# Kernel tuning notes

Hardware: AMD Instinct MI355X
Metric: run time of the kernel (lower is better)

The kernel has to match this reference:

```python
import jax, jax.numpy as jnp
import numpy as np

L, T, F, DIM = 16, 16384, 2, 3
N_MIN, N_MAX = 16.0, 512.0
N_PTS = 262144
# torch code builds np.int32 primes [1, 2654435761, 805459861]; 2654435761 wraps to -1640531535.
# Since T is a power of two, int32 wraparound multiply/xor followed by nonnegative mod T gives
# bit-identical indices to the int64 torch computation.
PIS = jnp.array([1, -1640531535, 805459861], dtype=jnp.int32)
# corner ordering from get_indices: corner k = a*4+b*2+c with a->dim0, b->dim1, c->dim2
OFFS = jnp.array([[(k >> 2) & 1, (k >> 1) & 1, k & 1] for k in range(8)], dtype=jnp.float32)  # (8,3)


def setup_inputs() -> dict:
    key = jax.random.key(0)
    k1, k2 = jax.random.split(key)
    x = jax.random.uniform(k1, (N_PTS, DIM), dtype=jnp.float32)
    # nn.init.uniform_(weight, a=-1e-4, b=1e-4) for each of L tables of shape (T, F)
    embeddings = jax.random.uniform(k2, (L, T, F), minval=-1e-4, maxval=1e-4, dtype=jnp.float32)
    return {"x": x, "embeddings": embeddings}


def reference(x, embeddings):
    # per-level growth factor b = exp((log Nmax - log Nmin)/L); N_l = Nmin * b**l
    b = jnp.exp((jnp.log(N_MAX) - jnp.log(N_MIN)) / L)
    N_l = N_MIN * b ** jnp.arange(L, dtype=jnp.float32)                      # (L,)
    un_x = x[None, :, :] * N_l[:, None, None]                                # (L,N,3)  (mu=0, sigma=1)
    lo = jnp.floor(un_x)
    hi = jnp.ceil(un_x)
    d = hi - lo                                                              # (L,N,3)
    nz = d != 0
    diff = jnp.where(nz, (un_x - lo) / jnp.where(nz, d, 1.0), 0.0)           # (L,N,3)

    mask = OFFS.astype(bool)[None, None]                                     # (1,1,8,3)
    corners = jnp.where(mask, hi[:, :, None, :], lo[:, :, None, :])          # (L,N,8,3)
    ci = corners.astype(jnp.int32)
    prod = ci * PIS                                                          # (L,N,8,3) wrapping int32 mul
    idx = jnp.mod(prod[..., 0] ^ prod[..., 1] ^ prod[..., 2], T)             # (L,N,8)

    # per-level table gather: (L,T,F)[ (L,N,8) ] -> (L,N,8,F)
    feats = jax.vmap(lambda emb, i: emb[i])(embeddings, idx)

    # trilinear weights: prod over dims of (diff if corner bit else 1-diff)
    w = jnp.prod(jnp.where(mask, diff[:, :, None, :], 1.0 - diff[:, :, None, :]), axis=-1)  # (L,N,8)
    c = jnp.einsum('lnc,lncf->lnf', w, feats)                                # (L,N,F)
    return jnp.transpose(c, (1, 0, 2)).reshape(x.shape[0], L * F)            # (N, L*F)
```

## Files before the change

kernel.cpp:

```cpp
#include <hip/hip_runtime.h>
#include <stdint.h>

constexpr int L_LEVELS = 16;
constexpr int T_SIZE   = 16384;
constexpr int N_PTS    = 262144;

typedef _Float16 h2 __attribute__((ext_vector_type(2)));
typedef _Float16 h8 __attribute__((ext_vector_type(8)));

constexpr uint32_t P1_4 = 2654435761u * 4u;
constexpr uint32_t P2_4 = 805459861u * 4u;
constexpr uint32_t M4   = (T_SIZE - 1) * 4u;

__device__ __forceinline__ h2 lerp2(h2 a, h2 b, h2 t) {
    return a + t * (b - a);
}

template <bool DIRECT>
__global__ __launch_bounds__(512, 4) void hash_encode_lds(
    const float* __restrict__ x,
    const float* __restrict__ emb,
    void* __restrict__ dst_raw)
{
    __shared__ h2 tab[T_SIZE];

    const int l     = blockIdx.x & (L_LEVELS - 1);
    const int chunk = blockIdx.x >> 4;
    const int t     = threadIdx.x;
    const int n0    = chunk * 4096 + t * 8;

    {
        const float4* __restrict__ src =
            reinterpret_cast<const float4*>(emb + (size_t)l * T_SIZE * 2);
        h8* __restrict__ d8 = reinterpret_cast<h8*>(tab);
#pragma unroll
        for (int it = 0; it < 8; ++it) {
            const int i = it * 512 + t;
            float4 a = src[2 * i];
            float4 b = src[2 * i + 1];
            h8 w = { (_Float16)a.x, (_Float16)a.y, (_Float16)a.z, (_Float16)a.w,
                     (_Float16)b.x, (_Float16)b.y, (_Float16)b.z, (_Float16)b.w };
            d8[i] = w;
        }
    }

    union { float4 q[6]; float f[24]; } xs;
    {
        const float4* __restrict__ xv =
            reinterpret_cast<const float4*>(x + (size_t)n0 * 3);
#pragma unroll
        for (int i = 0; i < 6; ++i) xs.q[i] = xv[i];
    }

    __syncthreads();

    const float Nl = 16.0f * exp2f((float)l * 0.3125f);
    const char* __restrict__ tb = reinterpret_cast<const char*>(tab);

    union { h2 r[8]; float4 q[2]; } res;

#pragma unroll
    for (int p = 0; p < 8; ++p) {
        const float u0 = xs.f[3 * p + 0] * Nl;
        const float u1 = xs.f[3 * p + 1] * Nl;
        const float u2 = xs.f[3 * p + 2] * Nl;

        const float fl0 = floorf(u0), fl1 = floorf(u1), fl2 = floorf(u2);
        const float df0 = u0 - fl0, df1 = u1 - fl1, df2 = u2 - fl2;

        const uint32_t q0 = ((uint32_t)(int32_t)fl0) << 2;
        const uint32_t q1 = ((uint32_t)(int32_t)fl1) * P1_4;
        const uint32_t q2 = ((uint32_t)(int32_t)fl2) * P2_4;
        const uint32_t d0 = (q0 ^ (q0 + 4u))   & M4;
        const uint32_t d1 = (q1 ^ (q1 + P1_4)) & M4;
        const uint32_t d2 = (q2 ^ (q2 + P2_4)) & M4;

        uint32_t off = (q0 ^ q1 ^ q2) & M4;

        constexpr int gray[8] = {0, 1, 3, 2, 6, 7, 5, 4};
        h2 f[8];
#pragma unroll
        for (int j = 0; j < 8; ++j) {
            f[gray[j]] = *reinterpret_cast<const h2*>(tb + off);
            if (j < 7) {
                const int tog = gray[j] ^ gray[j + 1];
                off ^= (tog == 4) ? d0 : (tog == 2) ? d1 : d2;
            }
        }

        const _Float16 h0 = (_Float16)df0, h1 = (_Float16)df1, hv2 = (_Float16)df2;
        const h2 t0 = {h0, h0}, t1 = {h1, h1}, t2 = {hv2, hv2};
        h2 e0 = lerp2(f[0], f[1], t2);
        h2 e1 = lerp2(f[2], f[3], t2);
        h2 e2 = lerp2(f[4], f[5], t2);
        h2 e3 = lerp2(f[6], f[7], t2);
        h2 g0 = lerp2(e0, e1, t1);
        h2 g1 = lerp2(e2, e3, t1);
        res.r[p] = lerp2(g0, g1, t0);
    }

    if (DIRECT) {
        float2* out = reinterpret_cast<float2*>(dst_raw);
#pragma unroll
        for (int p = 0; p < 8; ++p)
            out[(size_t)(n0 + p) * L_LEVELS + l] =
                make_float2((float)res.r[p].x, (float)res.r[p].y);
    } else {
        float4* ws4 = reinterpret_cast<float4*>(
            reinterpret_cast<h2*>(dst_raw) + (size_t)l * N_PTS + n0);
        ws4[0] = res.q[0];
        ws4[1] = res.q[1];
    }
}

__global__ __launch_bounds__(256) void transpose_lnf_nlf(
    const h2* __restrict__ ws,
    float2* __restrict__ out)
{
    __shared__ h2 tile[L_LEVELS][257];
    const int t    = threadIdx.x;
    const int base = blockIdx.x * 256;

#pragma unroll
    for (int l = 0; l < L_LEVELS; ++l)
        tile[l][t] = ws[(size_t)l * N_PTS + base + t];
    __syncthreads();

#pragma unroll
    for (int i = 0; i < L_LEVELS; ++i) {
        const int flat = i * 256 + t;
        const int p = flat >> 4;
        const int l = flat & 15;
        h2 v = tile[l][p];
        out[(size_t)base * L_LEVELS + flat] =
            make_float2((float)v.x, (float)v.y);
    }
}

extern "C" void kernel_launch(void* const* d_in, const int* in_sizes, int n_in,
                              void* d_out, int out_size, void* d_ws, size_t ws_size,
                              hipStream_t stream) {
    const float* x   = (const float*)d_in[0];
    const float* emb = (const float*)d_in[1];

    const size_t ws_needed = (size_t)N_PTS * L_LEVELS * sizeof(h2);

    if (ws_size >= ws_needed) {
        hash_encode_lds<false><<<1024, 512, 0, stream>>>(x, emb, d_ws);
        transpose_lnf_nlf<<<N_PTS / 256, 256, 0, stream>>>((const h2*)d_ws,
                                                           (float2*)d_out);
    } else {
        hash_encode_lds<true><<<1024, 512, 0, stream>>>(x, emb, d_out);
    }
}
```

Measured before the change: 86.83 us.

## Pre-convert tables to fp16, process two levels per block, vectorize transpose stores

Adds a small kernel that converts the embedding tables to fp16 once into workspace. The encode kernel then loads two levels' tables per 1024-thread block and reuses each point's coordinates across both levels. The transpose is widened to handle 512 points per block and write float4s that pack two levels. This trades an extra launch and workspace traffic for less redundant x loading and conversion, plus wider output stores; occupancy changes with the 128KB LDS per block.

```diff
diff --git a/kernel.cpp b/kernel.cpp
--- a/kernel.cpp
+++ b/kernel.cpp
@@ -6,6 +6,7 @@
 constexpr int N_PTS    = 262144;
 
 typedef _Float16 h2 __attribute__((ext_vector_type(2)));
+typedef _Float16 h4 __attribute__((ext_vector_type(4)));
 typedef _Float16 h8 __attribute__((ext_vector_type(8)));
 
 constexpr uint32_t P1_4 = 2654435761u * 4u;
@@ -16,11 +17,138 @@
     return a + t * (b - a);
 }
 
-template <bool DIRECT>
-__global__ __launch_bounds__(512, 4) void hash_encode_lds(
+__global__ __launch_bounds__(256) void cvt_emb(
+    const float4* __restrict__ src, h4* __restrict__ dst)
+{
+    const int i = blockIdx.x * 256 + threadIdx.x;
+    const float4 v = src[i];
+    h4 w = { (_Float16)v.x, (_Float16)v.y, (_Float16)v.z, (_Float16)v.w };
+    dst[i] = w;
+}
+
+__global__ __launch_bounds__(1024, 4) void hash_encode_pair(
+    const float* __restrict__ x,
+    const h2* __restrict__ emb16,
+    h2* __restrict__ ws)
+{
+    __shared__ h2 tab[2][T_SIZE];
+
+    const int lp    = blockIdx.x & 7;
+    const int chunk = blockIdx.x >> 3;
+    const int t     = threadIdx.x;
+    const int n0    = chunk * 8192 + t * 8;
+
+    {
+        const float4* __restrict__ sA =
+            reinterpret_cast<const float4*>(emb16 + (size_t)lp * T_SIZE);
+        const float4* __restrict__ sB =
+            reinterpret_cast<const float4*>(emb16 + (size_t)(lp + 8) * T_SIZE);
+        float4* __restrict__ dA = reinterpret_cast<float4*>(tab[0]);
+        float4* __restrict__ dB = reinterpret_cast<float4*>(tab[1]);
+#pragma unroll
+        for (int it = 0; it < 4; ++it) {
+            dA[it * 1024 + t] = sA[it * 1024 + t];
+            dB[it * 1024 + t] = sB[it * 1024 + t];
+        }
+    }
+
+    union { float4 q[6]; float f[24]; } xs;
+    {
+        const float4* __restrict__ xv =
+            reinterpret_cast<const float4*>(x + (size_t)n0 * 3);
+#pragma unroll
+        for (int i = 0; i < 6; ++i) xs.q[i] = xv[i];
+    }
+
+    __syncthreads();
+
+#pragma unroll 1
+    for (int s = 0; s < 2; ++s) {
+        const int lv = lp + 8 * s;
+        const float Nl = 16.0f * exp2f((float)lv * 0.3125f);
+        const char* __restrict__ tb = reinterpret_cast<const char*>(tab[s]);
+
+        union { h2 r[8]; float4 q[2]; } res;
+
+#pragma unroll
+        for (int p = 0; p < 8; ++p) {
+            const float u0 = xs.f[3 * p + 0] * Nl;
+            const float u1 = xs.f[3 * p + 1] * Nl;
+            const float u2 = xs.f[3 * p + 2] * Nl;
+
+            const float fl0 = floorf(u0), fl1 = floorf(u1), fl2 = floorf(u2);
+            const float df0 = u0 - fl0, df1 = u1 - fl1, df2 = u2 - fl2;
+
+            const uint32_t q0 = ((uint32_t)(int32_t)fl0) << 2;
+            const uint32_t q1 = ((uint32_t)(int32_t)fl1) * P1_4;
+            const uint32_t q2 = ((uint32_t)(int32_t)fl2) * P2_4;
+            const uint32_t d0 = (q0 ^ (q0 + 4u))   & M4;
+            const uint32_t d1 = (q1 ^ (q1 + P1_4)) & M4;
+            const uint32_t d2 = (q2 ^ (q2 + P2_4)) & M4;
+
+            uint32_t off = (q0 ^ q1 ^ q2) & M4;
+
+            constexpr int gray[8] = {0, 1, 3, 2, 6, 7, 5, 4};
+            h2 f[8];
+#pragma unroll
+            for (int j = 0; j < 8; ++j) {
+                f[gray[j]] = *reinterpret_cast<const h2*>(tb + off);
+                if (j < 7) {
+                    const int tog = gray[j] ^ gray[j + 1];
+                    off ^= (tog == 4) ? d0 : (tog == 2) ? d1 : d2;
+                }
+            }
+
+            const _Float16 h0 = (_Float16)df0, h1 = (_Float16)df1,
+                           hz = (_Float16)df2;
+            const h2 t0 = {h0, h0}, t1 = {h1, h1}, t2 = {hz, hz};
+            h2 e0 = lerp2(f[0], f[1], t2);
+            h2 e1 = lerp2(f[2], f[3], t2);
+            h2 e2 = lerp2(f[4], f[5], t2);
+            h2 e3 = lerp2(f[6], f[7], t2);
+            h2 g0 = lerp2(e0, e1, t1);
+            h2 g1 = lerp2(e2, e3, t1);
+            res.r[p] = lerp2(g0, g1, t0);
+        }
+
+        float4* ws4 = reinterpret_cast<float4*>(ws + (size_t)lv * N_PTS + n0);
+        ws4[0] = res.q[0];
+        ws4[1] = res.q[1];
+    }
+}
+
+__global__ __launch_bounds__(256) void transpose_lnf_nlf(
+    const h2* __restrict__ ws,
+    float4* __restrict__ out4)
+{
+    __shared__ h2 tile[L_LEVELS][514];
+    const int t    = threadIdx.x;
+    const int base = blockIdx.x * 512;
+
+#pragma unroll
+    for (int l = 0; l < L_LEVELS; ++l) {
+        const float2 v = *reinterpret_cast<const float2*>(
+            ws + (size_t)l * N_PTS + base + 2 * t);
+        *reinterpret_cast<float2*>(&tile[l][2 * t]) = v;
+    }
+    __syncthreads();
+
+#pragma unroll
+    for (int i = 0; i < L_LEVELS; ++i) {
+        const int flat = i * 256 + t;
+        const int p  = flat >> 3;
+        const int lp = flat & 7;
+        h2 a = tile[2 * lp][p];
+        h2 b = tile[2 * lp + 1][p];
+        float4 o = { (float)a.x, (float)a.y, (float)b.x, (float)b.y };
+        out4[(size_t)(base + p) * 8 + lp] = o;
+    }
+}
+
+__global__ __launch_bounds__(512, 4) void hash_encode_direct(
     const float* __restrict__ x,
     const float* __restrict__ emb,
-    void* __restrict__ dst_raw)
+    float2* __restrict__ out)
 {
     __shared__ h2 tab[T_SIZE];
 
@@ -43,7 +171,6 @@
             d8[i] = w;
         }
     }
-
     union { float4 q[6]; float f[24]; } xs;
     {
         const float4* __restrict__ xv =
@@ -51,32 +178,25 @@
 #pragma unroll
         for (int i = 0; i < 6; ++i) xs.q[i] = xv[i];
     }
-
     __syncthreads();
 
     const float Nl = 16.0f * exp2f((float)l * 0.3125f);
     const char* __restrict__ tb = reinterpret_cast<const char*>(tab);
-
-    union { h2 r[8]; float4 q[2]; } res;
 
 #pragma unroll
     for (int p = 0; p < 8; ++p) {
         const float u0 = xs.f[3 * p + 0] * Nl;
         const float u1 = xs.f[3 * p + 1] * Nl;
         const float u2 = xs.f[3 * p + 2] * Nl;
-
         const float fl0 = floorf(u0), fl1 = floorf(u1), fl2 = floorf(u2);
         const float df0 = u0 - fl0, df1 = u1 - fl1, df2 = u2 - fl2;
-
         const uint32_t q0 = ((uint32_t)(int32_t)fl0) << 2;
         const uint32_t q1 = ((uint32_t)(int32_t)fl1) * P1_4;
         const uint32_t q2 = ((uint32_t)(int32_t)fl2) * P2_4;
         const uint32_t d0 = (q0 ^ (q0 + 4u))   & M4;
         const uint32_t d1 = (q1 ^ (q1 + P1_4)) & M4;
         const uint32_t d2 = (q2 ^ (q2 + P2_4)) & M4;
-
         uint32_t off = (q0 ^ q1 ^ q2) & M4;
-
         constexpr int gray[8] = {0, 1, 3, 2, 6, 7, 5, 4};
         h2 f[8];
 #pragma unroll
@@ -87,53 +207,17 @@
                 off ^= (tog == 4) ? d0 : (tog == 2) ? d1 : d2;
             }
         }
-
-        const _Float16 h0 = (_Float16)df0, h1 = (_Float16)df1, hv2 = (_Float16)df2;
-        const h2 t0 = {h0, h0}, t1 = {h1, h1}, t2 = {hv2, hv2};
+        const _Float16 h0 = (_Float16)df0, h1 = (_Float16)df1, hz = (_Float16)df2;
+        const h2 t0 = {h0, h0}, t1 = {h1, h1}, t2 = {hz, hz};
         h2 e0 = lerp2(f[0], f[1], t2);
         h2 e1 = lerp2(f[2], f[3], t2);
         h2 e2 = lerp2(f[4], f[5], t2);
         h2 e3 = lerp2(f[6], f[7], t2);
         h2 g0 = lerp2(e0, e1, t1);
         h2 g1 = lerp2(e2, e3, t1);
-        res.r[p] = lerp2(g0, g1, t0);
-    }
-
-    if (DIRECT) {
-        float2* out = reinterpret_cast<float2*>(dst_raw);
-#pragma unroll
-        for (int p = 0; p < 8; ++p)
-            out[(size_t)(n0 + p) * L_LEVELS + l] =
-                make_float2((float)res.r[p].x, (float)res.r[p].y);
-    } else {
-        float4* ws4 = reinterpret_cast<float4*>(
-            reinterpret_cast<h2*>(dst_raw) + (size_t)l * N_PTS + n0);
-        ws4[0] = res.q[0];
-        ws4[1] = res.q[1];
-    }
-}
-
-__global__ __launch_bounds__(256) void transpose_lnf_nlf(
-    const h2* __restrict__ ws,
-    float2* __restrict__ out)
-{
-    __shared__ h2 tile[L_LEVELS][257];
-    const int t    = threadIdx.x;
-    const int base = blockIdx.x * 256;
-
-#pragma unroll
-    for (int l = 0; l < L_LEVELS; ++l)
-        tile[l][t] = ws[(size_t)l * N_PTS + base + t];
-    __syncthreads();
-
-#pragma unroll
-    for (int i = 0; i < L_LEVELS; ++i) {
-        const int flat = i * 256 + t;
-        const int p = flat >> 4;
-        const int l = flat & 15;
-        h2 v = tile[l][p];
-        out[(size_t)base * L_LEVELS + flat] =
-            make_float2((float)v.x, (float)v.y);
+        h2 r  = lerp2(g0, g1, t0);
+        out[(size_t)(n0 + p) * L_LEVELS + l] =
+            make_float2((float)r.x, (float)r.y);
     }
 }
 
@@ -143,13 +227,19 @@
     const float* x   = (const float*)d_in[0];
     const float* emb = (const float*)d_in[1];
 
-    const size_t ws_needed = (size_t)N_PTS * L_LEVELS * sizeof(h2);
-
-    if (ws_size >= ws_needed) {
-        hash_encode_lds<false><<<1024, 512, 0, stream>>>(x, emb, d_ws);
-        transpose_lnf_nlf<<<N_PTS / 256, 256, 0, stream>>>((const h2*)d_ws,
-                                                           (float2*)d_out);
+    const size_t ws_arr_bytes = (size_t)N_PTS * L_LEVELS * sizeof(h2);
+    const size_t emb16_bytes  = (size_t)L_LEVELS * T_SIZE * sizeof(h2);
+
+    if (ws_size >= ws_arr_bytes + emb16_bytes) {
+        h2* ws    = (h2*)d_ws;
+        h2* emb16 = (h2*)((char*)d_ws + ws_arr_bytes);
+
+        cvt_emb<<<512, 256, 0, stream>>>(
+            (const float4*)emb, (h4*)emb16);
+        hash_encode_pair<<<256, 1024, 0, stream>>>(x, emb16, ws);
+        transpose_lnf_nlf<<<N_PTS / 512, 256, 0, stream>>>(
+            ws, (float4*)d_out);
     } else {
-        hash_encode_lds<true><<<1024, 512, 0, stream>>>(x, emb, d_out);
-    }
-}
+        hash_encode_direct<<<1024, 512, 0, stream>>>(x, emb, (float2*)d_out);
+    }
+}
```

After: 88.09 us. About the same (+1.4%).
